# Performance work log

Measured on AMD Instinct MI355X. Metric: run time of the kernel, lower is better.

## Reference

```python
import jax, jax.numpy as jnp
import numpy as np
from jax.scipy.linalg import expm

N_WIRES = 9
N_LAYERS = 4
EMBED = 512
BATCH = 64
D = 2 ** N_WIRES
P = N_WIRES * N_LAYERS * 2  # gate angles per sample


def _apply_gate(st, g, w):
    # st: (D, 2,...,2) complex64; apply 2x2 gate g on wire w
    st = jnp.moveaxis(st, 1 + w, -1)
    st = st @ g.T  # new[a] = sum_b g[a,b] old[b]
    return jnp.moveaxis(st, -1, 1 + w)


def _apply_cnot(st, c, t):
    st = jnp.moveaxis(st, (1 + c, 1 + t), (-2, -1))
    st = jnp.concatenate([st[..., 0:1, :], st[..., 1:2, ::-1]], axis=-2)
    return jnp.moveaxis(st, (-2, -1), (1 + c, 1 + t))


def _build_unitary(params):
    # simulate circuit on all D basis states at once (identity input)
    st = jnp.eye(D, dtype=jnp.complex64).reshape((D,) + (2,) * N_WIRES)
    idx = 0
    for _ in range(N_LAYERS):
        for w in range(N_WIRES):
            thy = params[idx]
            thz = params[idx + 1]
            idx += 2
            c = jnp.cos(thy * 0.5).astype(jnp.complex64)
            s = jnp.sin(thy * 0.5).astype(jnp.complex64)
            ry = jnp.stack([jnp.stack([c, -s]), jnp.stack([s, c])])
            ep = jnp.exp(0.5j * thz.astype(jnp.complex64))  # exp(i*thz/2)
            zero = jnp.zeros((), jnp.complex64)
            rz = jnp.stack([jnp.stack([jnp.conj(ep), zero]), jnp.stack([zero, ep])])
            st = _apply_gate(st, rz @ ry, w)  # Ry then Rz, fused
        for w in range(N_WIRES - 1):
            st = _apply_cnot(st, w, w + 1)
        st = _apply_cnot(st, N_WIRES - 1, 0)  # ring entangler (n_wires>1)
    # row index = input basis state i -> column i of U; take real part
    return jnp.real(st.reshape(D, D)).T


def _forward(t, w1, b1, w2, b2):
    h = jax.nn.silu(t[:, None] @ w1 + b1)          # (B, EMBED)
    params = h @ w2 + b2                            # (B, P)
    p_sg = jax.lax.stop_gradient(params)            # torch uses .detach() for the circuit
    U_stack = jax.vmap(_build_unitary)(p_sg)        # (B, D, D)
    B = t.shape[0]
    A = jnp.zeros((B, D * D), params.dtype).at[:, :P].set(params).reshape(B, D, D)
    A_skew = (A - jnp.swapaxes(A, -1, -2)) * 0.01
    U_diff = jax.vmap(expm)(A_skew)                 # (B, D, D)
    return jnp.einsum('bij,bjk->bik', U_stack, U_diff)


def setup_inputs() -> dict:
    key = jax.random.key(0)
    k_t, k1, kb1, k2, kb2 = jax.random.split(key, 5)
    t = jax.random.normal(k_t, (BATCH,), jnp.float32)
    w1 = jax.random.normal(k1, (1, EMBED), jnp.float32)
    b1 = jax.random.normal(kb1, (EMBED,), jnp.float32) * 0.1
    w2 = jax.random.normal(k2, (EMBED, P), jnp.float32) / np.sqrt(EMBED)
    b2 = jax.random.normal(kb2, (P,), jnp.float32) * 0.1
    return {"t": t, "w1": w1, "b1": b1, "w2": w2, "b2": b2}


def reference(t, w1, b1, w2, b2):
    return _forward(t, w1, b1, w2, b2)
```

## Files before the change

kernel.cpp:

```cpp
#include <hip/hip_runtime.h>
#include <math.h>


#define PSTRIDE 2560
#define GD_OFF  0
#define SC_OFF  144
#define L_OFF(l) (160 + (l)*256)
#define V_OFF   1184
#define W_OFF   1280
#define C0_OFF  1792

__device__ __forceinline__ float2 cmul(float2 a, float2 b){
  return make_float2(fmaf(a.x, b.x, -a.y*b.y), fmaf(a.x, b.y, a.y*b.x));
}

__device__ __forceinline__ float2 pk_fma_s_lo(float2 s2, float2 b, float2 c){
  float2 d;
  asm("v_pk_fma_f32 %0, %1, %2, %3 op_sel:[0,0,0] op_sel_hi:[0,1,1]"
      : "=v"(d) : "s"(s2), "v"(b), "v"(c));
  return d;
}
__device__ __forceinline__ float2 pk_mul_s_hi(float2 s2, float2 b){
  float2 d;
  asm("v_pk_mul_f32 %0, %1, %2 op_sel:[1,0] op_sel_hi:[1,1]"
      : "=v"(d) : "s"(s2), "v"(b));
  return d;
}
__device__ __forceinline__ float2 pk_fma_vs_lo(float2 a, float2 b, float2 c){
  float2 d;
  asm("v_pk_fma_f32 %0, %1, %2, %3 op_sel:[0,0,0] op_sel_hi:[0,1,1]"
      : "=v"(d) : "v"(a), "s"(b), "v"(c));
  return d;
}
__device__ __forceinline__ float2 pk_mul_vs_hi(float2 a, float2 b){
  float2 d;
  asm("v_pk_mul_f32 %0, %1, %2 op_sel:[1,0] op_sel_hi:[1,1]"
      : "=v"(d) : "v"(a), "s"(b));
  return d;
}
__device__ __forceinline__ float2 pk_fma_vv_lo(float2 a, float2 b, float2 c){
  float2 d;
  asm("v_pk_fma_f32 %0, %1, %2, %3 op_sel:[0,0,0] op_sel_hi:[0,1,1]"
      : "=v"(d) : "v"(a), "v"(b), "v"(c));
  return d;
}
__device__ __forceinline__ float2 pk_mul_vv_hi(float2 a, float2 b){
  float2 d;
  asm("v_pk_mul_f32 %0, %1, %2 op_sel:[1,0] op_sel_hi:[1,1]"
      : "=v"(d) : "v"(a), "v"(b));
  return d;
}
__device__ __forceinline__ float2 pk_swapneg(float2 c, float2 n){
  float2 d;
  asm("v_pk_mul_f32 %0, %1, %2 op_sel:[1,0] op_sel_hi:[0,1]"
      : "=v"(d) : "v"(c), "v"(n));
  return d;
}

__device__ __forceinline__ int Fperm(int x){
  int S = x ^ (x >> 1); S ^= S >> 2; S ^= S >> 4; S ^= S >> 8;
  return (S & 0xFF) | ((((x >> 8) ^ S) & 1) << 8);
}
__device__ __forceinline__ int physmap(int x){ return x ^ ((x >> 4) & 15); }

template<int STRIDE, bool UNIF>
__device__ __forceinline__ void apply_rot(float2 amp[8], const float* rp){
  const float2 R0 = ((const float2*)rp)[0];
  const float2 R1 = ((const float2*)rp)[1];
  #pragma unroll
  for (int b = 0; b < 8; ++b){
    if (b & STRIDE) continue;
    const float2 u = amp[b], v = amp[b + STRIDE];
    if constexpr (UNIF){
      amp[b]          = pk_fma_s_lo(R0, u, pk_mul_s_hi(R0, v));
      amp[b + STRIDE] = pk_fma_s_lo(R1, u, pk_mul_s_hi(R1, v));
    } else {
      amp[b]          = pk_fma_vv_lo(R0, u, pk_mul_vv_hi(R0, v));
      amp[b + STRIDE] = pk_fma_vv_lo(R1, u, pk_mul_vv_hi(R1, v));
    }
  }
}

template<bool UNIF>
__device__ __forceinline__ void run_layer(float2* __restrict__ S,
    const float* __restrict__ lb, const int lane,
    const int base1, const int base2, const int base3, const int baseF,
    const float2 NEG1P1){
  float2 amp[8];
  #pragma unroll
  for (int j = 0; j < 8; ++j) amp[j] = S[base1 ^ j];
  apply_rot<4, UNIF>(amp, lb + 6*4);
  apply_rot<2, UNIF>(amp, lb + 7*4);
  apply_rot<1, UNIF>(amp, lb + 8*4);
  #pragma unroll
  for (int j = 0; j < 8; ++j) S[base1 ^ j] = amp[j];
  #pragma unroll
  for (int j = 0; j < 8; ++j) amp[j] = S[base2 ^ ((j << 3) ^ (j >> 1))];
  apply_rot<4, UNIF>(amp, lb + 3*4);
  apply_rot<2, UNIF>(amp, lb + 4*4);
  apply_rot<1, UNIF>(amp, lb + 5*4);
  #pragma unroll
  for (int j = 0; j < 8; ++j) S[base2 ^ ((j << 3) ^ (j >> 1))] = amp[j];
  #pragma unroll
  for (int j = 0; j < 8; ++j) amp[j] = S[base3 ^ ((j << 6) ^ ((4*j) & 15))];
  apply_rot<4, UNIF>(amp, lb + 0*4);
  apply_rot<2, UNIF>(amp, lb + 1*4);
  apply_rot<1, UNIF>(amp, lb + 2*4);
  {
    const float2 A  = *(const float2*)(lb + 128 + lane*2);
    const float2 A2 = pk_swapneg(A, NEG1P1);
    #pragma unroll
    for (int j = 0; j < 8; ++j)
      amp[j] = pk_fma_vv_lo(amp[j], A, pk_mul_vv_hi(amp[j], A2));
    #pragma unroll
    for (int j = 0; j < 8; ++j){
      const float2 P = *(const float2*)(lb + 64 + j*4);
      const float2 Q = *(const float2*)(lb + 64 + j*4 + 2);
      if constexpr (UNIF)
        amp[j] = pk_fma_vs_lo(amp[j], P, pk_mul_vs_hi(amp[j], Q));
      else
        amp[j] = pk_fma_vv_lo(amp[j], P, pk_mul_vv_hi(amp[j], Q));
    }
  }
  #pragma unroll
  for (int j = 0; j < 8; ++j) S[baseF ^ physmap(Fperm(j << 6))] = amp[j];
}

__global__ __launch_bounds__(576)
void prep_kernel(const float* __restrict__ t,  const float* __restrict__ w1,
                 const float* __restrict__ b1, const float* __restrict__ w2,
                 const float* __restrict__ b2, float* __restrict__ prep){
  __shared__ float sh[512];
  __shared__ float part[8][72];
  __shared__ float spar[72];
  __shared__ float tl[4][256];
  __shared__ float ssc[3];
  __shared__ __align__(16) float2 vst[2][512];
  const int s = blockIdx.x;
  const float ts = t[s];
  for (int k = threadIdx.x; k < 512; k += 576){
    const float z = fmaf(ts, w1[k], b1[k]);
    sh[k] = z / (1.f + expf(-z));
  }
  __syncthreads();
  {
    const int p = threadIdx.x % 72, c = threadIdx.x / 72;
    float acc = 0.f;
    const int k0 = c*64;
    for (int k = k0; k < k0 + 64; ++k) acc = fmaf(sh[k], w2[k*72 + p], acc);
    part[c][p] = acc;
  }
  __syncthreads();
  if (threadIdx.x < 72){
    const int p = threadIdx.x;
    float acc = b2[p];
    #pragma unroll
    for (int c = 0; c < 8; ++c) acc += part[c][p];
    spar[p] = acc;
  }
  __syncthreads();
  float* pb = prep + (size_t)s*PSTRIDE;
  const int tid = threadIdx.x;
  if (tid < 256){
    const int l = tid >> 6, m = tid & 63;
    float2 acc = make_float2(1.f, 0.f);
    #pragma unroll
    for (int w = 3; w < 9; ++w){
      const float thz = spar[2*(9*l + w) + 1];
      float zi, zr; sincosf(0.5f*thz, &zi, &zr);
      const int bit = (m >> (8 - w)) & 1;
      acc = cmul(acc, make_float2(zr, bit ? zi : -zi));
    }
    pb[L_OFF(l) + 128 + 2*m]     = acc.x;
    pb[L_OFF(l) + 128 + 2*m + 1] = acc.y;
    tl[l][128 + 2*m]     = acc.x;
    tl[l][128 + 2*m + 1] = acc.y;
  } else if (tid < 288){
    const int q = tid - 256, l = q >> 3, j = q & 7;
    float2 acc = make_float2(1.f, 0.f);
    #pragma unroll
    for (int w = 0; w < 3; ++w){
      const float thz = spar[2*(9*l + w) + 1];
      float zi, zr; sincosf(0.5f*thz, &zi, &zr);
      const int bit = (j >> (2 - w)) & 1;
      acc = cmul(acc, make_float2(zr, bit ? zi : -zi));
    }
    float* o = pb + L_OFF(l) + 64 + j*4;
    o[0] = acc.x; o[1] = acc.y; o[2] = -acc.y; o[3] = acc.x;
    float* o2 = &tl[l][64 + j*4];
    o2[0] = acc.x; o2[1] = acc.y; o2[2] = -acc.y; o2[3] = acc.x;
  } else if (tid < 324){
    const int q = tid - 288, l = q / 9, w = q - l*9;
    const float thy = spar[2*(9*l + w)];
    float sy, cy; sincosf(0.5f*thy, &sy, &cy);
    float* o = pb + L_OFF(l) + w*4;
    o[0] = cy; o[1] = -sy; o[2] = sy; o[3] = cy;
    float* o2 = &tl[l][w*4];
    o2[0] = cy; o2[1] = -sy; o2[2] = sy; o2[3] = cy;
  } else if (tid < 333){
    const int w = tid - 324;
    const float thy = spar[2*w], thz = spar[2*w + 1];
    float sy, cy, zi, zr;
    sincosf(0.5f*thy, &sy, &cy);
    sincosf(0.5f*thz, &zi, &zr);
    const float gr[4] = { zr*cy, -zr*sy, zr*sy, zr*cy };
    const float gi[4] = { -zi*cy, zi*sy, zi*sy, zi*cy };
    float* o = pb + GD_OFF + w*16;
    #pragma unroll
    for (int e = 0; e < 4; ++e){
      o[e*4+0] = gr[e]; o[e*4+1] = gi[e]; o[e*4+2] = -gi[e]; o[e*4+3] = gr[e];
    }
  } else if (tid < 405){
    const int j = tid - 333;
    pb[V_OFF + j] = (j == 0) ? 0.f : 0.01f*spar[j];
  } else if (tid == 405){
    float th2 = 0.f;
    for (int j = 1; j < 72; ++j){ const float v = 0.01f*spar[j]; th2 = fmaf(v, v, th2); }
    const float th = sqrtf(th2);
    float alpha, beta;
    if (th > 1e-6f){
      alpha = sinf(th)/th;
      const float s2 = sinf(0.5f*th);
      beta = 2.f*s2*s2/th2;
    } else { alpha = 1.f - th2/6.f; beta = 0.5f; }
    pb[SC_OFF+0] = cosf(th);
    pb[SC_OFF+1] = alpha;
    pb[SC_OFF+2] = beta;
    ssc[0] = cosf(th); ssc[1] = alpha; ssc[2] = beta;
  }
  __syncthreads();
  if (tid < 128){
    const int wv = tid >> 6, lane = tid & 63;
    float2* const S = vst[wv];
    const float2 NEG1P1 = make_float2(-1.f, 1.f);
    const int base1 = (lane << 3) ^ ((lane >> 1) & 15);
    const int hq = lane >> 3, lq = lane & 7;
    const int base2 = (hq << 6) ^ ((hq << 2) & 15) ^ lq;
    const int base3 = lane ^ (lane >> 4);
    const int baseF = physmap(Fperm(lane));
    #pragma unroll
    for (int j = 0; j < 8; ++j){
      const int x = (lane << 3) + j;
      float re;
      if (wv == 0) re = (x == 0) ? 1.f : 0.f;
      else         re = (x >= 1 && x < 72) ? 0.01f*spar[x] : 0.f;
      S[base1 ^ j] = make_float2(re, 0.f);
    }
    #pragma unroll
    for (int L = 0; L < 4; ++L)
      run_layer<false>(S, &tl[L][0], lane, base1, base2, base3, baseF, NEG1P1);
  }
  __syncthreads();
  if (tid < 512){
    const int a  = tid;
    const int pa = a ^ ((a >> 4) & 15);
    const float u0 = vst[0][pa].x;
    const float uv = vst[1][pa].x;
    pb[W_OFF  + a] = fmaf(ssc[1], u0, -ssc[2]*uv);
    pb[C0_OFF + a] = fmaf(ssc[0], u0, -ssc[1]*uv);
  }
}

__global__ __launch_bounds__(512, 8)
void sim_kernel(const float* __restrict__ prep, float* __restrict__ out){
  __shared__ __align__(16) float2 st[8][512];
  const int s    = blockIdx.x & 63;
  const int cb   = blockIdx.x >> 6;
  const int wid  = threadIdx.x >> 6;
  const int lane = threadIdx.x & 63;
  const int col  = cb*8 + wid;
  const float* gp = prep + (size_t)s*PSTRIDE;
  float2* const S = st[wid];
  const float2 NEG1P1 = make_float2(-1.f, 1.f);

  float2 amp[8];
  {
    float2 base = make_float2(1.f, 0.f);
    #pragma unroll
    for (int w = 0; w < 6; ++w){
      const int xb = (lane >> (5 - w)) & 1;
      const int ib = (col  >> (8 - w)) & 1;
      const float4 gd = *(const float4*)(gp + GD_OFF + w*16 + (xb*2 + ib)*4);
      const float2 d1 = make_float2(gd.x, gd.y);
      const float2 d2 = make_float2(gd.z, gd.w);
      base = pk_fma_vv_lo(base, d1, pk_mul_vv_hi(base, d2));
    }
    const int i6 = (col >> 2) & 1, i7 = (col >> 1) & 1, i8 = col & 1;
    float2 g6[2]; float4 g7d[2], g8d[2];
    #pragma unroll
    for (int r = 0; r < 2; ++r){
      g6[r]  = *(const float2*)(gp + GD_OFF + 6*16 + (r*2 + i6)*4);
      g7d[r] = *(const float4*)(gp + GD_OFF + 7*16 + (r*2 + i7)*4);
      g8d[r] = *(const float4*)(gp + GD_OFF + 8*16 + (r*2 + i8)*4);
    }
    float2 g67[4];
    #pragma unroll
    for (int a = 0; a < 2; ++a){
      #pragma unroll
      for (int b = 0; b < 2; ++b){
        const float2 d1 = make_float2(g7d[b].x, g7d[b].y);
        const float2 d2 = make_float2(g7d[b].z, g7d[b].w);
        g67[a*2+b] = pk_fma_vv_lo(g6[a], d1, pk_mul_vv_hi(g6[a], d2));
      }
    }
    const float2 bd2 = pk_swapneg(base, NEG1P1);
    #pragma unroll
    for (int j = 0; j < 8; ++j){
      const float4 g8 = g8d[j & 1];
      const float2 e1 = make_float2(g8.x, g8.y);
      const float2 e2 = make_float2(g8.z, g8.w);
      const float2 T  = pk_fma_vv_lo(g67[j >> 1], e1, pk_mul_vv_hi(g67[j >> 1], e2));
      amp[j] = pk_fma_vv_lo(T, base, pk_mul_vv_hi(T, bd2));
    }
    const int bFI = physmap(Fperm(lane << 3));
    #pragma unroll
    for (int j = 0; j < 8; ++j) S[bFI ^ physmap(Fperm(j))] = amp[j];
  }

  const int base1 = (lane << 3) ^ ((lane >> 1) & 15);
  const int hq = lane >> 3, lq = lane & 7;
  const int base2 = (hq << 6) ^ ((hq << 2) & 15) ^ lq;
  const int base3 = lane ^ (lane >> 4);
  const int baseF = physmap(Fperm(lane));

  run_layer<true>(S, gp + L_OFF(1), lane, base1, base2, base3, baseF, NEG1P1);
  run_layer<true>(S, gp + L_OFF(2), lane, base1, base2, base3, baseF, NEG1P1);
  run_layer<true>(S, gp + L_OFF(3), lane, base1, base2, base3, baseF, NEG1P1);

  __syncthreads();
  const float* wt  = gp + W_OFF;
  const float* c0t = gp + C0_OFF;
  const float* vt  = gp + V_OFF;
  #pragma unroll
  for (int rep = 0; rep < 2; ++rep){
    const int a  = (threadIdx.x >> 1) + rep*256;
    const int q  = threadIdx.x & 1;
    const int pa = a ^ ((a >> 4) & 15);
    float4 vv;
    vv.x = st[q*4 + 0][pa].x;
    vv.y = st[q*4 + 1][pa].x;
    vv.z = st[q*4 + 2][pa].x;
    vv.w = st[q*4 + 3][pa].x;
    if (cb < 9){
      const float  wa = wt[a];
      const float4 vj = *(const float4*)(vt + cb*8 + q*4);
      vv.x = fmaf(wa, vj.x, vv.x);
      vv.y = fmaf(wa, vj.y, vv.y);
      vv.z = fmaf(wa, vj.z, vv.z);
      vv.w = fmaf(wa, vj.w, vv.w);
      if ((cb | q) == 0) vv.x = c0t[a];
    }
    *(float4*)&out[(size_t)s*262144 + (size_t)a*512 + cb*8 + q*4] = vv;
  }
}

extern "C" void kernel_launch(void* const* d_in, const int* in_sizes, int n_in,
                              void* d_out, int out_size, void* d_ws, size_t ws_size,
                              hipStream_t stream){
  const float* t  = (const float*)d_in[0];
  const float* w1 = (const float*)d_in[1];
  const float* b1 = (const float*)d_in[2];
  const float* w2 = (const float*)d_in[3];
  const float* b2 = (const float*)d_in[4];
  float* out  = (float*)d_out;
  float* prep = (float*)d_ws;
  prep_kernel<<<64,   576, 0, stream>>>(t, w1, b1, w2, b2, prep);
  sim_kernel <<<4096, 512, 0, stream>>>(prep, out);
}
```

Measured before the change: 144.9 us.

## Process two state columns per wavefront with float4 amplitudes in sim kernel

Each wavefront in sim_kernel now simulates two adjacent columns of the unitary at once, packing their amplitudes into float4. This halves the thread count per block from 512 to 256, so each loaded rotation coefficient and LDS index computation is reused across two columns, and LDS traffic moves in wider 16-byte accesses. The cost is more registers per thread (launch bounds 256,6) and a different LDS layout for the final output gather, which could lower occupancy or add bank conflicts.

```diff
diff --git a/kernel.cpp b/kernel.cpp
--- a/kernel.cpp
+++ b/kernel.cpp
@@ -57,55 +57,55 @@
   return d;
 }
 
+__device__ __forceinline__ float2 f4lo(float4 v){ return make_float2(v.x, v.y); }
+__device__ __forceinline__ float2 f4hi(float4 v){ return make_float2(v.z, v.w); }
+__device__ __forceinline__ float4 mk4(float2 a, float2 b){
+  float4 r; r.x = a.x; r.y = a.y; r.z = b.x; r.w = b.y; return r;
+}
+
 __device__ __forceinline__ int Fperm(int x){
   int S = x ^ (x >> 1); S ^= S >> 2; S ^= S >> 4; S ^= S >> 8;
   return (S & 0xFF) | ((((x >> 8) ^ S) & 1) << 8);
 }
 __device__ __forceinline__ int physmap(int x){ return x ^ ((x >> 4) & 15); }
 
-template<int STRIDE, bool UNIF>
-__device__ __forceinline__ void apply_rot(float2 amp[8], const float* rp){
+template<int STRIDE>
+__device__ __forceinline__ void apply_rot2(float2 amp[8], const float* rp){
   const float2 R0 = ((const float2*)rp)[0];
   const float2 R1 = ((const float2*)rp)[1];
   #pragma unroll
   for (int b = 0; b < 8; ++b){
     if (b & STRIDE) continue;
     const float2 u = amp[b], v = amp[b + STRIDE];
-    if constexpr (UNIF){
-      amp[b]          = pk_fma_s_lo(R0, u, pk_mul_s_hi(R0, v));
-      amp[b + STRIDE] = pk_fma_s_lo(R1, u, pk_mul_s_hi(R1, v));
-    } else {
-      amp[b]          = pk_fma_vv_lo(R0, u, pk_mul_vv_hi(R0, v));
-      amp[b + STRIDE] = pk_fma_vv_lo(R1, u, pk_mul_vv_hi(R1, v));
-    }
-  }
-}
-
-template<bool UNIF>
-__device__ __forceinline__ void run_layer(float2* __restrict__ S,
+    amp[b]          = pk_fma_vv_lo(R0, u, pk_mul_vv_hi(R0, v));
+    amp[b + STRIDE] = pk_fma_vv_lo(R1, u, pk_mul_vv_hi(R1, v));
+  }
+}
+
+__device__ __forceinline__ void run_layer2(float2* __restrict__ S,
     const float* __restrict__ lb, const int lane,
     const int base1, const int base2, const int base3, const int baseF,
     const float2 NEG1P1){
   float2 amp[8];
   #pragma unroll
   for (int j = 0; j < 8; ++j) amp[j] = S[base1 ^ j];
-  apply_rot<4, UNIF>(amp, lb + 6*4);
-  apply_rot<2, UNIF>(amp, lb + 7*4);
-  apply_rot<1, UNIF>(amp, lb + 8*4);
+  apply_rot2<4>(amp, lb + 6*4);
+  apply_rot2<2>(amp, lb + 7*4);
+  apply_rot2<1>(amp, lb + 8*4);
   #pragma unroll
   for (int j = 0; j < 8; ++j) S[base1 ^ j] = amp[j];
   #pragma unroll
   for (int j = 0; j < 8; ++j) amp[j] = S[base2 ^ ((j << 3) ^ (j >> 1))];
-  apply_rot<4, UNIF>(amp, lb + 3*4);
-  apply_rot<2, UNIF>(amp, lb + 4*4);
-  apply_rot<1, UNIF>(amp, lb + 5*4);
+  apply_rot2<4>(amp, lb + 3*4);
+  apply_rot2<2>(amp, lb + 4*4);
+  apply_rot2<1>(amp, lb + 5*4);
   #pragma unroll
   for (int j = 0; j < 8; ++j) S[base2 ^ ((j << 3) ^ (j >> 1))] = amp[j];
   #pragma unroll
   for (int j = 0; j < 8; ++j) amp[j] = S[base3 ^ ((j << 6) ^ ((4*j) & 15))];
-  apply_rot<4, UNIF>(amp, lb + 0*4);
-  apply_rot<2, UNIF>(amp, lb + 1*4);
-  apply_rot<1, UNIF>(amp, lb + 2*4);
+  apply_rot2<4>(amp, lb + 0*4);
+  apply_rot2<2>(amp, lb + 1*4);
+  apply_rot2<1>(amp, lb + 2*4);
   {
     const float2 A  = *(const float2*)(lb + 128 + lane*2);
     const float2 A2 = pk_swapneg(A, NEG1P1);
@@ -116,10 +116,69 @@
     for (int j = 0; j < 8; ++j){
       const float2 P = *(const float2*)(lb + 64 + j*4);
       const float2 Q = *(const float2*)(lb + 64 + j*4 + 2);
-      if constexpr (UNIF)
-        amp[j] = pk_fma_vs_lo(amp[j], P, pk_mul_vs_hi(amp[j], Q));
-      else
-        amp[j] = pk_fma_vv_lo(amp[j], P, pk_mul_vv_hi(amp[j], Q));
+      amp[j] = pk_fma_vv_lo(amp[j], P, pk_mul_vv_hi(amp[j], Q));
+    }
+  }
+  #pragma unroll
+  for (int j = 0; j < 8; ++j) S[baseF ^ physmap(Fperm(j << 6))] = amp[j];
+}
+
+template<int STRIDE>
+__device__ __forceinline__ void apply_rot4(float4 amp[8], const float* rp){
+  const float2 R0 = ((const float2*)rp)[0];
+  const float2 R1 = ((const float2*)rp)[1];
+  #pragma unroll
+  for (int b = 0; b < 8; ++b){
+    if (b & STRIDE) continue;
+    const float2 ulo = f4lo(amp[b]),        uhi = f4hi(amp[b]);
+    const float2 vlo = f4lo(amp[b+STRIDE]), vhi = f4hi(amp[b+STRIDE]);
+    amp[b]          = mk4(pk_fma_s_lo(R0, ulo, pk_mul_s_hi(R0, vlo)),
+                          pk_fma_s_lo(R0, uhi, pk_mul_s_hi(R0, vhi)));
+    amp[b + STRIDE] = mk4(pk_fma_s_lo(R1, ulo, pk_mul_s_hi(R1, vlo)),
+                          pk_fma_s_lo(R1, uhi, pk_mul_s_hi(R1, vhi)));
+  }
+}
+
+__device__ __forceinline__ void run_layer4(float4* __restrict__ S,
+    const float* __restrict__ lb, const int lane,
+    const int base1, const int base2, const int base3, const int baseF,
+    const float2 NEG1P1){
+  float4 amp[8];
+  #pragma unroll
+  for (int j = 0; j < 8; ++j) amp[j] = S[base1 ^ j];
+  apply_rot4<4>(amp, lb + 6*4);
+  apply_rot4<2>(amp, lb + 7*4);
+  apply_rot4<1>(amp, lb + 8*4);
+  #pragma unroll
+  for (int j = 0; j < 8; ++j) S[base1 ^ j] = amp[j];
+  #pragma unroll
+  for (int j = 0; j < 8; ++j) amp[j] = S[base2 ^ ((j << 3) ^ (j >> 1))];
+  apply_rot4<4>(amp, lb + 3*4);
+  apply_rot4<2>(amp, lb + 4*4);
+  apply_rot4<1>(amp, lb + 5*4);
+  #pragma unroll
+  for (int j = 0; j < 8; ++j) S[base2 ^ ((j << 3) ^ (j >> 1))] = amp[j];
+  #pragma unroll
+  for (int j = 0; j < 8; ++j) amp[j] = S[base3 ^ ((j << 6) ^ ((4*j) & 15))];
+  apply_rot4<4>(amp, lb + 0*4);
+  apply_rot4<2>(amp, lb + 1*4);
+  apply_rot4<1>(amp, lb + 2*4);
+  {
+    const float2 A  = *(const float2*)(lb + 128 + lane*2);
+    const float2 A2 = pk_swapneg(A, NEG1P1);
+    #pragma unroll
+    for (int j = 0; j < 8; ++j){
+      const float2 lo = f4lo(amp[j]), hi = f4hi(amp[j]);
+      amp[j] = mk4(pk_fma_vv_lo(lo, A, pk_mul_vv_hi(lo, A2)),
+                   pk_fma_vv_lo(hi, A, pk_mul_vv_hi(hi, A2)));
+    }
+    #pragma unroll
+    for (int j = 0; j < 8; ++j){
+      const float2 P = *(const float2*)(lb + 64 + j*4);
+      const float2 Q = *(const float2*)(lb + 64 + j*4 + 2);
+      const float2 lo = f4lo(amp[j]), hi = f4hi(amp[j]);
+      amp[j] = mk4(pk_fma_vs_lo(lo, P, pk_mul_vs_hi(lo, Q)),
+                   pk_fma_vs_lo(hi, P, pk_mul_vs_hi(hi, Q)));
     }
   }
   #pragma unroll
@@ -248,7 +307,7 @@
     }
     #pragma unroll
     for (int L = 0; L < 4; ++L)
-      run_layer<false>(S, &tl[L][0], lane, base1, base2, base3, baseF, NEG1P1);
+      run_layer2(S, &tl[L][0], lane, base1, base2, base3, baseF, NEG1P1);
   }
   __syncthreads();
   if (tid < 512){
@@ -261,56 +320,57 @@
   }
 }
 
-__global__ __launch_bounds__(512, 8)
+__global__ __launch_bounds__(256, 6)
 void sim_kernel(const float* __restrict__ prep, float* __restrict__ out){
-  __shared__ __align__(16) float2 st[8][512];
+  __shared__ __align__(16) float4 st[4][512];
   const int s    = blockIdx.x & 63;
   const int cb   = blockIdx.x >> 6;
   const int wid  = threadIdx.x >> 6;
   const int lane = threadIdx.x & 63;
-  const int col  = cb*8 + wid;
   const float* gp = prep + (size_t)s*PSTRIDE;
-  float2* const S = st[wid];
+  float4* const S = st[wid];
   const float2 NEG1P1 = make_float2(-1.f, 1.f);
 
-  float2 amp[8];
+  float4 amp[8];
   {
     float2 base = make_float2(1.f, 0.f);
     #pragma unroll
     for (int w = 0; w < 6; ++w){
       const int xb = (lane >> (5 - w)) & 1;
-      const int ib = (col  >> (8 - w)) & 1;
+      const int ib = (cb   >> (5 - w)) & 1;
       const float4 gd = *(const float4*)(gp + GD_OFF + w*16 + (xb*2 + ib)*4);
       const float2 d1 = make_float2(gd.x, gd.y);
       const float2 d2 = make_float2(gd.z, gd.w);
       base = pk_fma_vv_lo(base, d1, pk_mul_vv_hi(base, d2));
     }
-    const int i6 = (col >> 2) & 1, i7 = (col >> 1) & 1, i8 = col & 1;
-    float2 g6[2]; float4 g7d[2], g8d[2];
+    const int i6 = (wid >> 1) & 1, i7 = wid & 1;
+    float2 g6[2], g7[2];
+    float4 g8d[4];
     #pragma unroll
     for (int r = 0; r < 2; ++r){
-      g6[r]  = *(const float2*)(gp + GD_OFF + 6*16 + (r*2 + i6)*4);
-      g7d[r] = *(const float4*)(gp + GD_OFF + 7*16 + (r*2 + i7)*4);
-      g8d[r] = *(const float4*)(gp + GD_OFF + 8*16 + (r*2 + i8)*4);
+      g6[r]      = *(const float2*)(gp + GD_OFF + 6*16 + (r*2 + i6)*4);
+      g7[r]      = *(const float2*)(gp + GD_OFF + 7*16 + (r*2 + i7)*4);
+      g8d[r*2+0] = *(const float4*)(gp + GD_OFF + 8*16 + (r*2 + 0)*4);
+      g8d[r*2+1] = *(const float4*)(gp + GD_OFF + 8*16 + (r*2 + 1)*4);
     }
     float2 g67[4];
     #pragma unroll
-    for (int a = 0; a < 2; ++a){
+    for (int a = 0; a < 2; ++a)
       #pragma unroll
-      for (int b = 0; b < 2; ++b){
-        const float2 d1 = make_float2(g7d[b].x, g7d[b].y);
-        const float2 d2 = make_float2(g7d[b].z, g7d[b].w);
-        g67[a*2+b] = pk_fma_vv_lo(g6[a], d1, pk_mul_vv_hi(g6[a], d2));
-      }
-    }
+      for (int b = 0; b < 2; ++b)
+        g67[a*2+b] = cmul(g6[a], g7[b]);
     const float2 bd2 = pk_swapneg(base, NEG1P1);
     #pragma unroll
     for (int j = 0; j < 8; ++j){
-      const float4 g8 = g8d[j & 1];
-      const float2 e1 = make_float2(g8.x, g8.y);
-      const float2 e2 = make_float2(g8.z, g8.w);
-      const float2 T  = pk_fma_vv_lo(g67[j >> 1], e1, pk_mul_vv_hi(g67[j >> 1], e2));
-      amp[j] = pk_fma_vv_lo(T, base, pk_mul_vv_hi(T, bd2));
+      const float2 T  = g67[j >> 1];
+      const float4 ga = g8d[(j & 1)*2 + 0];
+      const float4 gb = g8d[(j & 1)*2 + 1];
+      const float2 Ta = pk_fma_vv_lo(T, make_float2(ga.x, ga.y),
+                                     pk_mul_vv_hi(T, make_float2(ga.z, ga.w)));
+      const float2 Tb = pk_fma_vv_lo(T, make_float2(gb.x, gb.y),
+                                     pk_mul_vv_hi(T, make_float2(gb.z, gb.w)));
+      amp[j] = mk4(pk_fma_vv_lo(Ta, base, pk_mul_vv_hi(Ta, bd2)),
+                   pk_fma_vv_lo(Tb, base, pk_mul_vv_hi(Tb, bd2)));
     }
     const int bFI = physmap(Fperm(lane << 3));
     #pragma unroll
@@ -323,24 +383,25 @@
   const int base3 = lane ^ (lane >> 4);
   const int baseF = physmap(Fperm(lane));
 
-  run_layer<true>(S, gp + L_OFF(1), lane, base1, base2, base3, baseF, NEG1P1);
-  run_layer<true>(S, gp + L_OFF(2), lane, base1, base2, base3, baseF, NEG1P1);
-  run_layer<true>(S, gp + L_OFF(3), lane, base1, base2, base3, baseF, NEG1P1);
+  run_layer4(S, gp + L_OFF(1), lane, base1, base2, base3, baseF, NEG1P1);
+  run_layer4(S, gp + L_OFF(2), lane, base1, base2, base3, baseF, NEG1P1);
+  run_layer4(S, gp + L_OFF(3), lane, base1, base2, base3, baseF, NEG1P1);
 
   __syncthreads();
   const float* wt  = gp + W_OFF;
   const float* c0t = gp + C0_OFF;
   const float* vt  = gp + V_OFF;
-  #pragma unroll
-  for (int rep = 0; rep < 2; ++rep){
-    const int a  = (threadIdx.x >> 1) + rep*256;
-    const int q  = threadIdx.x & 1;
+  const int q  = threadIdx.x & 1;
+  const int a0 = threadIdx.x >> 1;
+  #pragma unroll
+  for (int rep = 0; rep < 4; ++rep){
+    const int a  = a0 + rep*128;
     const int pa = a ^ ((a >> 4) & 15);
     float4 vv;
-    vv.x = st[q*4 + 0][pa].x;
-    vv.y = st[q*4 + 1][pa].x;
-    vv.z = st[q*4 + 2][pa].x;
-    vv.w = st[q*4 + 3][pa].x;
+    vv.x = st[q*2 + 0][pa].x;
+    vv.y = st[q*2 + 0][pa].z;
+    vv.z = st[q*2 + 1][pa].x;
+    vv.w = st[q*2 + 1][pa].z;
     if (cb < 9){
       const float  wa = wt[a];
       const float4 vj = *(const float4*)(vt + cb*8 + q*4);
@@ -365,5 +426,5 @@
   float* out  = (float*)d_out;
   float* prep = (float*)d_ws;
   prep_kernel<<<64,   576, 0, stream>>>(t, w1, b1, w2, b2, prep);
-  sim_kernel <<<4096, 512, 0, stream>>>(prep, out);
-}
+  sim_kernel <<<4096, 256, 0, stream>>>(prep, out);
+}
```

Result: no change. 145.2 us (+0.2%).
